# Performance work log

Hardware: AMD Instinct MI355X
Metric: run time of the kernel (lower is better)

The kernel has to match this reference:

```python
import jax, jax.numpy as jnp
import numpy as np

# Network dimensions (match init_kwargs)
N_IN, N_HID, N_OUT = 2048, 8192, 1024
N = N_IN + N_HID + N_OUT
BATCH = 512


def setup_inputs() -> dict:
    key = jax.random.key(0)
    k_w, k_b, k_x = jax.random.split(key, 3)
    # GraphNet._init_connections: Xavier-ish std based on (n_inputs + n_outputs)
    std = (2.0 / (N_IN + N_OUT)) ** 0.5
    W = jax.random.normal(k_w, (N, N), dtype=jnp.float32) * std
    # mask: inputs -> hidden, hidden -> outputs (fixed 3-level DAG)
    mask = jnp.zeros((N, N), dtype=jnp.float32)
    mask = mask.at[:N_IN, N_IN:N_IN + N_HID].set(1.0)
    mask = mask.at[N_IN:N_IN + N_HID, N_IN + N_HID:].set(1.0)
    # bias is zero-init in the module; use small random values so it is exercised
    bias = jax.random.normal(k_b, (N,), dtype=jnp.float32) * 0.01
    x = jax.random.normal(k_x, (BATCH, N_IN), dtype=jnp.float32)
    return {"x": x, "W": W, "bias": bias, "mask": mask}


def reference(x, W, bias, mask):
    # Faithful translation of GraphNet.forward for the canonical 3-level
    # topology produced by _init_connections/_compute_levels:
    #   level 0: input nodes [0, N_IN)
    #   level 1: hidden nodes [N_IN, N_IN+N_HID)  -> ReLU
    #   level 2: output nodes [N_IN+N_HID, N)     -> identity (OUTPUT type)
    W_eff = W * mask                       # [N, N] masked adjacency
    B = x.shape[0]
    h = jnp.zeros((B, N), dtype=x.dtype).at[:, :N_IN].set(x)
    # level 1 (hidden): pre_act = h @ W_eff[:, idx] + bias[idx]; ReLU
    pre_h = h @ W_eff[:, N_IN:N_IN + N_HID] + bias[N_IN:N_IN + N_HID]
    h = h.at[:, N_IN:N_IN + N_HID].set(jax.nn.relu(pre_h))
    # level 2 (outputs): pre-activation only (node_type == OUTPUT -> no ReLU)
    pre_o = h @ W_eff[:, N_IN + N_HID:] + bias[N_IN + N_HID:]
    return pre_o                            # h[:, output_indices]
```

## Files before the change

kernel.cpp:

```cpp
#include <hip/hip_runtime.h>

#define N_IN 2048
#define N_HID 8192
#define N_OUT 1024
#define NTOT 11264

typedef __attribute__((ext_vector_type(4))) float f32x4;
typedef __attribute__((ext_vector_type(4))) short short4v;
typedef __attribute__((ext_vector_type(8))) short short8v;
typedef __attribute__((ext_vector_type(2))) unsigned u32x2;

__device__ inline short f2bf(float f) {
    unsigned u = __float_as_uint(f);
    return (short)((u + 0x7fffu + ((u >> 16) & 1u)) >> 16);
}

__device__ inline float bf2f(short s) {
    return __uint_as_float(((unsigned)(unsigned short)s) << 16);
}

__device__ inline unsigned cvt_pk_bf16(float lo, float hi) {
    unsigned r;
    asm("v_cvt_pk_bf16_f32 %0, %1, %2" : "=v"(r) : "v"(lo), "v"(hi));
    return r;
}

__device__ inline int perm64(int c) {
    return (c & 32) + (((c >> 2) & 3) << 3) + (((c >> 4) & 1) << 2) + (c & 3);
}

__device__ inline void gload_lds16(const void* g, void* l) {
    __builtin_amdgcn_global_load_lds(
        (const __attribute__((address_space(1))) unsigned int*)g,
        (__attribute__((address_space(3))) unsigned int*)l, 16, 0, 0);
}

__global__ __launch_bounds__(256) void cvt_x(
    const float* __restrict__ x, short* __restrict__ xb)
{
    const int i = blockIdx.x * 256 + threadIdx.x;
    const f32x4 v = *reinterpret_cast<const f32x4*>(x + (size_t)i * 4);
    u32x2 s;
    s[0] = cvt_pk_bf16(v[0], v[1]);
    s[1] = cvt_pk_bf16(v[2], v[3]);
    const int c0  = (i * 4) & (N_IN - 1);
    const int p   = (c0 & ~63) + perm64(c0 & 63);
    const size_t row = (size_t)(i >> 9);
    *reinterpret_cast<u32x2*>(xb + row * N_IN + p) = s;
}

template<bool FUSE>
__global__ __launch_bounds__(512, 2) void gemm_bf16(
    const short* __restrict__ A,
    const float* __restrict__ W,
    const float* __restrict__ bias,
    short* __restrict__ hOut,
    short* __restrict__ pOut,
    int lda, int nt, int wrow0, int wcol0)
{
    __shared__ __align__(16) short As[4][128 * 64];
    __shared__ __align__(16) short Bs[2][128][72];

    const int bid = blockIdx.x;
    const int xcd = bid & 7;
    const int j   = bid >> 3;
    int bx, by, bz;
    if (FUSE) {
        bx = xcd * 8 + (j >> 2);
        by = j & 3;
        bz = 0;
    } else {
        const int xz = xcd * 8 + (j >> 2);
        bx = xz & 7;
        bz = xz >> 3;
        by = j & 3;
    }

    const int t    = threadIdx.x;
    const int lane = t & 63;
    const int wid  = t >> 6;
    const int wr   = wid >> 2;
    const int wc   = wid & 3;
    const int brow = by * 128;
    const int bcol = bx * 128;
    const int l15  = lane & 15;
    const int lg   = lane >> 4;
    const int ks   = bz * 1024;

    const int arow = lane >> 3;
    const int asw  = ((lane & 7) * 16) ^ (arow << 4);

    const int nb   = (lane & 7) + 8 * (wid >> 1);
    const int kblk = ((lane >> 3) & 7) + 8 * (wid & 1);
    const int n0 = nb * 4, k0 = kblk * 4;
    const int p0 = perm64(k0);

    const char*  Abytes = (const char*)A;
    const size_t lda_b  = (size_t)lda * 2;

    f32x4 acc[4][2] = {};
    f32x4 bv0[4], bv1[4], bv2[4], bv3[4];

    const float* wp0 = &W[(size_t)(wrow0 + ks + k0) * NTOT + (wcol0 + bcol + n0)];

#define B_LOAD(TT, BV) { \
    const float* wp = wp0 + (size_t)(TT) * 64 * NTOT; \
    _Pragma("unroll") for (int jj = 0; jj < 4; ++jj) \
        BV[jj] = *reinterpret_cast<const f32x4*>(wp + (size_t)jj * NTOT); }

#define A_LOAD(TT) { \
    char* dst = (char*)As + ((TT) & 3) * 16384; \
    _Pragma("unroll") for (int i = 0; i < 2; ++i) { \
        const int c = wid * 2 + i; \
        gload_lds16(Abytes + (size_t)(brow + c * 8 + arow) * lda_b \
                          + (size_t)(ks + (TT) * 64) * 2 + asw, \
                    dst + c * 1024); } }

#define B_WRITE(TT, BV) { \
    short* bsb = &Bs[(TT) & 1][0][0]; \
    _Pragma("unroll") for (int i = 0; i < 4; ++i) { \
        u32x2 s; \
        s[0] = cvt_pk_bf16(BV[0][i], BV[1][i]); \
        s[1] = cvt_pk_bf16(BV[2][i], BV[3][i]); \
        *reinterpret_cast<u32x2*>(bsb + (n0 + i) * 72 + p0) = s; } }

#define COMPUTE(TT) { \
    const char*  ab = (const char*)As + ((TT) & 3) * 16384; \
    const short* bb = &Bs[(TT) & 1][0][0]; \
    short8v a[2][4], b[2][2]; \
    _Pragma("unroll") for (int g = 0; g < 2; ++g) { \
        const int koff = g * 64 + lg * 16; \
        _Pragma("unroll") for (int m = 0; m < 4; ++m) { \
            const int r = wr * 64 + m * 16 + l15; \
            a[g][m] = *reinterpret_cast<const short8v*>( \
                ab + ((r * 128 + koff) ^ ((r & 7) << 4))); } \
        _Pragma("unroll") for (int n = 0; n < 2; ++n) { \
            const int r = wc * 32 + n * 16 + l15; \
            b[g][n] = *reinterpret_cast<const short8v*>( \
                (const char*)(bb + r * 72) + koff); } } \
    __builtin_amdgcn_s_setprio(1); \
    _Pragma("unroll") for (int g = 0; g < 2; ++g) \
      _Pragma("unroll") for (int m = 0; m < 4; ++m) \
        _Pragma("unroll") for (int n = 0; n < 2; ++n) \
            acc[m][n] = __builtin_amdgcn_mfma_f32_16x16x32_bf16( \
                a[g][m], b[g][n], acc[m][n], 0, 0, 0); \
    __builtin_amdgcn_s_setprio(0); }

#define WAITV(N) { asm volatile("s_waitcnt vmcnt(" #N ")" ::: "memory"); \
                   __builtin_amdgcn_sched_barrier(0); }
#define BARRIER  { asm volatile("s_waitcnt lgkmcnt(0)" ::: "memory"); \
                   __builtin_amdgcn_sched_barrier(0); \
                   __builtin_amdgcn_s_barrier(); \
                   __builtin_amdgcn_sched_barrier(0); }

#define ITER(T, BVL, BVW) { \
    B_LOAD(T + 3, BVL); A_LOAD(T + 3); \
    WAITV(12); \
    B_WRITE(T + 1, BVW); \
    COMPUTE(T); \
    BARRIER; }

    B_LOAD(0, bv0); A_LOAD(0);
    B_LOAD(1, bv1); A_LOAD(1);
    B_LOAD(2, bv2); A_LOAD(2);
    WAITV(12);
    B_WRITE(0, bv0);
    BARRIER;

    for (int tt = 0; tt + 4 < nt; tt += 4) {
        ITER(tt,     bv3, bv1);
        ITER(tt + 1, bv0, bv2);
        ITER(tt + 2, bv1, bv3);
        ITER(tt + 3, bv2, bv0);
    }
    ITER(nt - 4, bv3, bv1);

    WAITV(6);
    B_WRITE(nt - 2, bv2);
    COMPUTE(nt - 3);
    BARRIER;
    WAITV(0);
    B_WRITE(nt - 1, bv3);
    COMPUTE(nt - 2);
    BARRIER;
    COMPUTE(nt - 1);

#undef B_LOAD
#undef A_LOAD
#undef B_WRITE
#undef COMPUTE
#undef WAITV
#undef BARRIER
#undef ITER

    if (FUSE) {
#pragma unroll
        for (int m = 0; m < 4; ++m) {
            const int row0 = brow + wr * 64 + m * 16 + lg * 4;
#pragma unroll
            for (int n = 0; n < 2; ++n) {
                const int col  = bcol + wc * 32 + n * 16 + l15;
                const int pcol = (col & ~63) + perm64(col & 63);
                const float bb = bias[N_IN + col];
#pragma unroll
                for (int q = 0; q < 4; ++q) {
                    float v = acc[m][n][q] + bb;
                    v = v > 0.f ? v : 0.f;
                    hOut[(size_t)(row0 + q) * N_HID + pcol] = f2bf(v);
                }
            }
        }
    } else {
        short* po = pOut + (size_t)bz * (512 * N_OUT);
#pragma unroll
        for (int m = 0; m < 4; ++m) {
            const int row0 = brow + wr * 64 + m * 16 + lg * 4;
#pragma unroll
            for (int n = 0; n < 2; ++n) {
                const int col = bcol + wc * 32 + n * 16 + l15;
#pragma unroll
                for (int q = 0; q < 4; ++q)
                    po[(size_t)(row0 + q) * N_OUT + col] = f2bf(acc[m][n][q]);
            }
        }
    }
}

__global__ __launch_bounds__(256) void reduce_bias(
    const short* __restrict__ part,
    const float* __restrict__ bias,
    float* __restrict__ out)
{
    const int idx = (blockIdx.x * 256 + threadIdx.x) * 4;
    f32x4 s = *reinterpret_cast<const f32x4*>(&bias[N_IN + N_HID + (idx & 1023)]);
#pragma unroll
    for (int sp = 0; sp < 8; ++sp) {
        const short4v p = *reinterpret_cast<const short4v*>(
            &part[(size_t)sp * 524288 + idx]);
#pragma unroll
        for (int jj = 0; jj < 4; ++jj) s[jj] += bf2f(p[jj]);
    }
    *reinterpret_cast<f32x4*>(&out[idx]) = s;
}

extern "C" void kernel_launch(void* const* d_in, const int* in_sizes, int n_in,
                              void* d_out, int out_size, void* d_ws, size_t ws_size,
                              hipStream_t stream) {
    const float* x    = (const float*)d_in[0];
    const float* W    = (const float*)d_in[1];
    const float* bias = (const float*)d_in[2];
    float* out = (float*)d_out;

    short* h    = (short*)d_ws;
    short* part = (short*)((char*)d_ws + (size_t)(8 << 20));
    short* xb   = (short*)((char*)d_ws + (size_t)(8 << 20));

    cvt_x<<<dim3(1024), dim3(256), 0, stream>>>(x, xb);

    gemm_bf16<true><<<dim3(256), dim3(512), 0, stream>>>(
        xb, W, bias, h, nullptr, N_IN, 32, 0, N_IN);

    gemm_bf16<false><<<dim3(256), dim3(512), 0, stream>>>(
        h, W, nullptr, nullptr, part, N_HID, 16, N_IN, N_IN + N_HID);

    reduce_bias<<<dim3(512), dim3(256), 0, stream>>>(part, bias, out);
}
```

Before: 66.24 us.

## Convert second-layer weights to bf16 inside first GEMM for cheaper loads

During the first GEMM, each block also reads a slice of the hidden-to-output fp32 weight block, converts it to bf16 and writes it to workspace. The second GEMM then loads these packed bf16 weights and skips per-tile conversion, halving its weight traffic. In exchange the first GEMM does extra fp32 reads and bf16 writes in its first 16 iterations. The path only runs when the workspace is at least 32 MB.

```diff
diff --git a/kernel.cpp b/kernel.cpp
--- a/kernel.cpp
+++ b/kernel.cpp
@@ -1,4 +1,5 @@
 #include <hip/hip_runtime.h>
+#include <type_traits>
 
 #define N_IN 2048
 #define N_HID 8192
@@ -49,13 +50,14 @@
     *reinterpret_cast<u32x2*>(xb + row * N_IN + p) = s;
 }
 
-template<bool FUSE>
+template<bool FUSE, bool BBF16>
 __global__ __launch_bounds__(512, 2) void gemm_bf16(
     const short* __restrict__ A,
     const float* __restrict__ W,
     const float* __restrict__ bias,
     short* __restrict__ hOut,
     short* __restrict__ pOut,
+    short* __restrict__ w2,
     int lda, int nt, int wrow0, int wcol0)
 {
     __shared__ __align__(16) short As[4][128 * 64];
@@ -98,15 +100,26 @@
     const char*  Abytes = (const char*)A;
     const size_t lda_b  = (size_t)lda * 2;
 
+    using BT = typename std::conditional<BBF16 && !FUSE, short4v, f32x4>::type;
+
     f32x4 acc[4][2] = {};
-    f32x4 bv0[4], bv1[4], bv2[4], bv3[4];
-
-    const float* wp0 = &W[(size_t)(wrow0 + ks + k0) * NTOT + (wcol0 + bcol + n0)];
+    BT bv0[4], bv1[4], bv2[4], bv3[4];
+
+    const char* bSrc;
+    size_t bStride;
+    if (BBF16 && !FUSE) {
+        bSrc = (const char*)(w2 + (size_t)(ks + k0) * 1024 + (bcol + n0));
+        bStride = 1024 * 2;
+    } else {
+        bSrc = (const char*)&W[(size_t)(wrow0 + ks + k0) * NTOT
+                               + (wcol0 + bcol + n0)];
+        bStride = (size_t)NTOT * 4;
+    }
 
 #define B_LOAD(TT, BV) { \
-    const float* wp = wp0 + (size_t)(TT) * 64 * NTOT; \
+    const char* wp = bSrc + (size_t)(TT) * 64 * bStride; \
     _Pragma("unroll") for (int jj = 0; jj < 4; ++jj) \
-        BV[jj] = *reinterpret_cast<const f32x4*>(wp + (size_t)jj * NTOT); }
+        BV[jj] = *reinterpret_cast<const BT*>(wp + (size_t)jj * bStride); }
 
 #define A_LOAD(TT) { \
     char* dst = (char*)As + ((TT) & 3) * 16384; \
@@ -120,9 +133,29 @@
     short* bsb = &Bs[(TT) & 1][0][0]; \
     _Pragma("unroll") for (int i = 0; i < 4; ++i) { \
         u32x2 s; \
-        s[0] = cvt_pk_bf16(BV[0][i], BV[1][i]); \
-        s[1] = cvt_pk_bf16(BV[2][i], BV[3][i]); \
+        if constexpr (BBF16 && !FUSE) { \
+            s[0] = (unsigned)(unsigned short)BV[0][i] \
+                 | ((unsigned)(unsigned short)BV[1][i] << 16); \
+            s[1] = (unsigned)(unsigned short)BV[2][i] \
+                 | ((unsigned)(unsigned short)BV[3][i] << 16); \
+        } else { \
+            s[0] = cvt_pk_bf16(BV[0][i], BV[1][i]); \
+            s[1] = cvt_pk_bf16(BV[2][i], BV[3][i]); \
+        } \
         *reinterpret_cast<u32x2*>(bsb + (n0 + i) * 72 + p0) = s; } }
+
+#define RIDERW(TT) { \
+    if constexpr (FUSE && BBF16) { \
+        if ((TT) < 16) { \
+            const int f4 = (bid << 13) + (TT) * 512 + t; \
+            const int rr = f4 >> 8; \
+            const int cc = (f4 & 255) << 2; \
+            const f32x4 wv = *reinterpret_cast<const f32x4*>( \
+                &W[(size_t)(N_IN + rr) * NTOT + (N_IN + N_HID + cc)]); \
+            u32x2 pk; \
+            pk[0] = cvt_pk_bf16(wv[0], wv[1]); \
+            pk[1] = cvt_pk_bf16(wv[2], wv[3]); \
+            *reinterpret_cast<u32x2*>(w2 + ((size_t)f4 << 2)) = pk; } } }
 
 #define COMPUTE(TT) { \
     const char*  ab = (const char*)As + ((TT) & 3) * 16384; \
@@ -157,6 +190,7 @@
     B_LOAD(T + 3, BVL); A_LOAD(T + 3); \
     WAITV(12); \
     B_WRITE(T + 1, BVW); \
+    RIDERW(T); \
     COMPUTE(T); \
     BARRIER; }
 
@@ -188,6 +222,7 @@
 #undef B_LOAD
 #undef A_LOAD
 #undef B_WRITE
+#undef RIDERW
 #undef COMPUTE
 #undef WAITV
 #undef BARRIER
@@ -254,14 +289,23 @@
     short* h    = (short*)d_ws;
     short* part = (short*)((char*)d_ws + (size_t)(8 << 20));
     short* xb   = (short*)((char*)d_ws + (size_t)(8 << 20));
+    short* w2b  = (short*)((char*)d_ws + (size_t)(16 << 20));
+
+    const bool big = ws_size >= ((size_t)32 << 20);
 
     cvt_x<<<dim3(1024), dim3(256), 0, stream>>>(x, xb);
 
-    gemm_bf16<true><<<dim3(256), dim3(512), 0, stream>>>(
-        xb, W, bias, h, nullptr, N_IN, 32, 0, N_IN);
-
-    gemm_bf16<false><<<dim3(256), dim3(512), 0, stream>>>(
-        h, W, nullptr, nullptr, part, N_HID, 16, N_IN, N_IN + N_HID);
+    if (big) {
+        gemm_bf16<true, true><<<dim3(256), dim3(512), 0, stream>>>(
+            xb, W, bias, h, nullptr, w2b, N_IN, 32, 0, N_IN);
+        gemm_bf16<false, true><<<dim3(256), dim3(512), 0, stream>>>(
+            h, W, nullptr, nullptr, part, w2b, N_HID, 16, N_IN, N_IN + N_HID);
+    } else {
+        gemm_bf16<true, false><<<dim3(256), dim3(512), 0, stream>>>(
+            xb, W, bias, h, nullptr, nullptr, N_IN, 32, 0, N_IN);
+        gemm_bf16<false, false><<<dim3(256), dim3(512), 0, stream>>>(
+            h, W, nullptr, nullptr, part, nullptr, N_HID, 16, N_IN, N_IN + N_HID);
+    }
 
     reduce_bias<<<dim3(512), dim3(256), 0, stream>>>(part, bias, out);
 }
```

Result: slower. 71.05 us (+7.3%).

## Retile second GEMM to 256x64 tiles with per-XCD split-K mapping

Applied to the files above, without the earlier changes.

Splits the templated GEMM into two specialized kernels. The output-layer GEMM now uses 256x64 block tiles with 8 waves in a 4x2 layout, so each fp32 W tile is re-read by fewer blocks and more of the redundant traffic falls on the cheaper bf16 activations. Block indices are remapped so each XCD handles one K-split slice, which is meant to keep that W slab local to one L2. The cost is a larger LDS footprint for A, which may limit occupancy, and the activation matrix is reloaded more often.

```diff
diff --git a/kernel.cpp b/kernel.cpp
--- a/kernel.cpp
+++ b/kernel.cpp
@@ -34,6 +34,13 @@
         (const __attribute__((address_space(1))) unsigned int*)g,
         (__attribute__((address_space(3))) unsigned int*)l, 16, 0, 0);
 }
+
+#define WAITV(N) { asm volatile("s_waitcnt vmcnt(" #N ")" ::: "memory"); \
+                   __builtin_amdgcn_sched_barrier(0); }
+#define BARRIER  { asm volatile("s_waitcnt lgkmcnt(0)" ::: "memory"); \
+                   __builtin_amdgcn_sched_barrier(0); \
+                   __builtin_amdgcn_s_barrier(); \
+                   __builtin_amdgcn_sched_barrier(0); }
 
 __global__ __launch_bounds__(256) void cvt_x(
     const float* __restrict__ x, short* __restrict__ xb)
@@ -49,14 +56,11 @@
     *reinterpret_cast<u32x2*>(xb + row * N_IN + p) = s;
 }
 
-template<bool FUSE>
-__global__ __launch_bounds__(512, 2) void gemm_bf16(
+__global__ __launch_bounds__(512, 2) void gemm1(
     const short* __restrict__ A,
     const float* __restrict__ W,
     const float* __restrict__ bias,
-    short* __restrict__ hOut,
-    short* __restrict__ pOut,
-    int lda, int nt, int wrow0, int wcol0)
+    short* __restrict__ hOut)
 {
     __shared__ __align__(16) short As[4][128 * 64];
     __shared__ __align__(16) short Bs[2][128][72];
@@ -64,17 +68,8 @@
     const int bid = blockIdx.x;
     const int xcd = bid & 7;
     const int j   = bid >> 3;
-    int bx, by, bz;
-    if (FUSE) {
-        bx = xcd * 8 + (j >> 2);
-        by = j & 3;
-        bz = 0;
-    } else {
-        const int xz = xcd * 8 + (j >> 2);
-        bx = xz & 7;
-        bz = xz >> 3;
-        by = j & 3;
-    }
+    const int bx  = xcd * 8 + (j >> 2);
+    const int by  = j & 3;
 
     const int t    = threadIdx.x;
     const int lane = t & 63;
@@ -85,7 +80,6 @@
     const int bcol = bx * 128;
     const int l15  = lane & 15;
     const int lg   = lane >> 4;
-    const int ks   = bz * 1024;
 
     const int arow = lane >> 3;
     const int asw  = ((lane & 7) * 16) ^ (arow << 4);
@@ -96,12 +90,12 @@
     const int p0 = perm64(k0);
 
     const char*  Abytes = (const char*)A;
-    const size_t lda_b  = (size_t)lda * 2;
+    const size_t lda_b  = (size_t)N_IN * 2;
 
     f32x4 acc[4][2] = {};
     f32x4 bv0[4], bv1[4], bv2[4], bv3[4];
 
-    const float* wp0 = &W[(size_t)(wrow0 + ks + k0) * NTOT + (wcol0 + bcol + n0)];
+    const float* wp0 = &W[(size_t)k0 * NTOT + (N_IN + bcol + n0)];
 
 #define B_LOAD(TT, BV) { \
     const float* wp = wp0 + (size_t)(TT) * 64 * NTOT; \
@@ -113,7 +107,7 @@
     _Pragma("unroll") for (int i = 0; i < 2; ++i) { \
         const int c = wid * 2 + i; \
         gload_lds16(Abytes + (size_t)(brow + c * 8 + arow) * lda_b \
-                          + (size_t)(ks + (TT) * 64) * 2 + asw, \
+                          + (size_t)((TT) * 64) * 2 + asw, \
                     dst + c * 1024); } }
 
 #define B_WRITE(TT, BV) { \
@@ -146,13 +140,6 @@
                 a[g][m], b[g][n], acc[m][n], 0, 0, 0); \
     __builtin_amdgcn_s_setprio(0); }
 
-#define WAITV(N) { asm volatile("s_waitcnt vmcnt(" #N ")" ::: "memory"); \
-                   __builtin_amdgcn_sched_barrier(0); }
-#define BARRIER  { asm volatile("s_waitcnt lgkmcnt(0)" ::: "memory"); \
-                   __builtin_amdgcn_sched_barrier(0); \
-                   __builtin_amdgcn_s_barrier(); \
-                   __builtin_amdgcn_sched_barrier(0); }
-
 #define ITER(T, BVL, BVW) { \
     B_LOAD(T + 3, BVL); A_LOAD(T + 3); \
     WAITV(12); \
@@ -167,6 +154,7 @@
     B_WRITE(0, bv0);
     BARRIER;
 
+    const int nt = 32;
     for (int tt = 0; tt + 4 < nt; tt += 4) {
         ITER(tt,     bv3, bv1);
         ITER(tt + 1, bv0, bv2);
@@ -189,39 +177,157 @@
 #undef A_LOAD
 #undef B_WRITE
 #undef COMPUTE
-#undef WAITV
-#undef BARRIER
 #undef ITER
 
-    if (FUSE) {
-#pragma unroll
-        for (int m = 0; m < 4; ++m) {
-            const int row0 = brow + wr * 64 + m * 16 + lg * 4;
-#pragma unroll
-            for (int n = 0; n < 2; ++n) {
-                const int col  = bcol + wc * 32 + n * 16 + l15;
-                const int pcol = (col & ~63) + perm64(col & 63);
-                const float bb = bias[N_IN + col];
-#pragma unroll
-                for (int q = 0; q < 4; ++q) {
-                    float v = acc[m][n][q] + bb;
-                    v = v > 0.f ? v : 0.f;
-                    hOut[(size_t)(row0 + q) * N_HID + pcol] = f2bf(v);
-                }
+#pragma unroll
+    for (int m = 0; m < 4; ++m) {
+        const int row0 = brow + wr * 64 + m * 16 + lg * 4;
+#pragma unroll
+        for (int n = 0; n < 2; ++n) {
+            const int col  = bcol + wc * 32 + n * 16 + l15;
+            const int pcol = (col & ~63) + perm64(col & 63);
+            const float bb = bias[N_IN + col];
+#pragma unroll
+            for (int q = 0; q < 4; ++q) {
+                float v = acc[m][n][q] + bb;
+                v = v > 0.f ? v : 0.f;
+                hOut[(size_t)(row0 + q) * N_HID + pcol] = f2bf(v);
             }
         }
-    } else {
-        short* po = pOut + (size_t)bz * (512 * N_OUT);
-#pragma unroll
-        for (int m = 0; m < 4; ++m) {
-            const int row0 = brow + wr * 64 + m * 16 + lg * 4;
-#pragma unroll
-            for (int n = 0; n < 2; ++n) {
-                const int col = bcol + wc * 32 + n * 16 + l15;
-#pragma unroll
-                for (int q = 0; q < 4; ++q)
-                    po[(size_t)(row0 + q) * N_OUT + col] = f2bf(acc[m][n][q]);
-            }
+    }
+}
+
+__global__ __launch_bounds__(512, 2) void gemm2(
+    const short* __restrict__ A,
+    const float* __restrict__ W,
+    short* __restrict__ pOut)
+{
+    __shared__ __align__(16) short As[4][256 * 64];
+    __shared__ __align__(16) short Bs[2][64][72];
+
+    const int bid = blockIdx.x;
+    const int bz  = bid & 7;
+    const int j   = bid >> 3;
+    const int bx  = j >> 1;
+    const int by  = j & 1;
+
+    const int t    = threadIdx.x;
+    const int lane = t & 63;
+    const int wid  = t >> 6;
+    const int wr   = wid >> 1;
+    const int wc   = wid & 1;
+    const int brow = by * 256;
+    const int bcol = bx * 64;
+    const int l15  = lane & 15;
+    const int lg   = lane >> 4;
+    const int ks   = bz * 1024;
+
+    const int arow = lane >> 3;
+    const int asw  = ((lane & 7) * 16) ^ (arow << 4);
+
+    const int k2 = (t >> 4) * 2;
+    const int n0 = (t & 15) * 4;
+    const int p2 = perm64(k2);
+
+    const char*  Abytes = (const char*)A;
+    const size_t lda_b  = (size_t)N_HID * 2;
+
+    f32x4 acc[4][2] = {};
+    f32x4 bv0[2], bv1[2], bv2[2], bv3[2];
+
+    const float* wp0 = &W[(size_t)(N_IN + ks + k2) * NTOT
+                          + (N_IN + N_HID + bcol + n0)];
+
+#define B_LOAD(TT, BV) { \
+    const float* wp = wp0 + (size_t)(TT) * 64 * NTOT; \
+    BV[0] = *reinterpret_cast<const f32x4*>(wp); \
+    BV[1] = *reinterpret_cast<const f32x4*>(wp + NTOT); }
+
+#define A_LOAD(TT) { \
+    char* dst = (char*)As + ((TT) & 3) * 32768; \
+    _Pragma("unroll") for (int i = 0; i < 4; ++i) { \
+        const int c = wid * 4 + i; \
+        gload_lds16(Abytes + (size_t)(brow + c * 8 + arow) * lda_b \
+                          + (size_t)(ks + (TT) * 64) * 2 + asw, \
+                    dst + c * 1024); } }
+
+#define B_WRITE(TT, BV) { \
+    short* bsb = &Bs[(TT) & 1][0][0]; \
+    _Pragma("unroll") for (int i = 0; i < 4; ++i) { \
+        unsigned s = cvt_pk_bf16(BV[0][i], BV[1][i]); \
+        *reinterpret_cast<unsigned*>(bsb + (n0 + i) * 72 + p2) = s; } }
+
+#define COMPUTE(TT) { \
+    const char*  ab = (const char*)As + ((TT) & 3) * 32768; \
+    const short* bb = &Bs[(TT) & 1][0][0]; \
+    short8v a[2][4], b[2][2]; \
+    _Pragma("unroll") for (int g = 0; g < 2; ++g) { \
+        const int koff = g * 64 + lg * 16; \
+        _Pragma("unroll") for (int m = 0; m < 4; ++m) { \
+            const int r = wr * 64 + m * 16 + l15; \
+            a[g][m] = *reinterpret_cast<const short8v*>( \
+                ab + ((r * 128 + koff) ^ ((r & 7) << 4))); } \
+        _Pragma("unroll") for (int n = 0; n < 2; ++n) { \
+            const int r = wc * 32 + n * 16 + l15; \
+            b[g][n] = *reinterpret_cast<const short8v*>( \
+                (const char*)(bb + r * 72) + koff); } } \
+    __builtin_amdgcn_s_setprio(1); \
+    _Pragma("unroll") for (int g = 0; g < 2; ++g) \
+      _Pragma("unroll") for (int m = 0; m < 4; ++m) \
+        _Pragma("unroll") for (int n = 0; n < 2; ++n) \
+            acc[m][n] = __builtin_amdgcn_mfma_f32_16x16x32_bf16( \
+                a[g][m], b[g][n], acc[m][n], 0, 0, 0); \
+    __builtin_amdgcn_s_setprio(0); }
+
+#define ITER(T, BVL, BVW) { \
+    B_LOAD(T + 3, BVL); A_LOAD(T + 3); \
+    WAITV(12); \
+    B_WRITE(T + 1, BVW); \
+    COMPUTE(T); \
+    BARRIER; }
+
+    B_LOAD(0, bv0); A_LOAD(0);
+    B_LOAD(1, bv1); A_LOAD(1);
+    B_LOAD(2, bv2); A_LOAD(2);
+    WAITV(12);
+    B_WRITE(0, bv0);
+    BARRIER;
+
+    const int nt = 16;
+    for (int tt = 0; tt + 4 < nt; tt += 4) {
+        ITER(tt,     bv3, bv1);
+        ITER(tt + 1, bv0, bv2);
+        ITER(tt + 2, bv1, bv3);
+        ITER(tt + 3, bv2, bv0);
+    }
+    ITER(nt - 4, bv3, bv1);
+
+    WAITV(6);
+    B_WRITE(nt - 2, bv2);
+    COMPUTE(nt - 3);
+    BARRIER;
+    WAITV(0);
+    B_WRITE(nt - 1, bv3);
+    COMPUTE(nt - 2);
+    BARRIER;
+    COMPUTE(nt - 1);
+
+#undef B_LOAD
+#undef A_LOAD
+#undef B_WRITE
+#undef COMPUTE
+#undef ITER
+
+    short* po = pOut + (size_t)bz * (512 * N_OUT);
+#pragma unroll
+    for (int m = 0; m < 4; ++m) {
+        const int row0 = brow + wr * 64 + m * 16 + lg * 4;
+#pragma unroll
+        for (int n = 0; n < 2; ++n) {
+            const int col = bcol + wc * 32 + n * 16 + l15;
+#pragma unroll
+            for (int q = 0; q < 4; ++q)
+                po[(size_t)(row0 + q) * N_OUT + col] = f2bf(acc[m][n][q]);
         }
     }
 }
@@ -257,11 +363,9 @@
 
     cvt_x<<<dim3(1024), dim3(256), 0, stream>>>(x, xb);
 
-    gemm_bf16<true><<<dim3(256), dim3(512), 0, stream>>>(
-        xb, W, bias, h, nullptr, N_IN, 32, 0, N_IN);
-
-    gemm_bf16<false><<<dim3(256), dim3(512), 0, stream>>>(
-        h, W, nullptr, nullptr, part, N_HID, 16, N_IN, N_IN + N_HID);
+    gemm1<<<dim3(256), dim3(512), 0, stream>>>(xb, W, bias, h);
+
+    gemm2<<<dim3(256), dim3(512), 0, stream>>>(h, W, part);
 
     reduce_bias<<<dim3(512), dim3(256), 0, stream>>>(part, bias, out);
 }
```

Result: no change. 66.74 us (+0.7%).
